# Optimization experiments

Hardware: AMD Instinct MI355X
Metric: run time of the kernel (lower is better)

Reference implementation:

```python
import jax, jax.numpy as jnp
import numpy as np
import math

N, S, D, C, CLASSES = 512, 256, 512, 1024, 1000


def setup_inputs() -> dict:
    key = jax.random.key(0)
    ks = jax.random.split(key, 9)
    q = jax.random.normal(ks[0], (N, D), dtype=jnp.float32)
    K = jax.random.normal(ks[1], (N, S, D), dtype=jnp.float32)
    V = jax.random.normal(ks[2], (N, S, D), dtype=jnp.float32)
    codebook = jax.random.normal(ks[3], (C, D), dtype=jnp.float32) / math.sqrt(D)
    Wq = jax.random.normal(ks[4], (D, D), dtype=jnp.float32) / math.sqrt(D)
    Wc = jax.random.normal(ks[5], (CLASSES, D), dtype=jnp.float32) / math.sqrt(D)
    bc = jnp.zeros((CLASSES,), dtype=jnp.float32)
    Wr = jax.random.normal(ks[6], (D, D), dtype=jnp.float32) / math.sqrt(D)
    br = jnp.zeros((D,), dtype=jnp.float32)
    return {"q": q, "K": K, "V": V, "codebook": codebook,
            "Wq": Wq, "Wc": Wc, "bc": bc, "Wr": Wr, "br": br}


def reference(q, K, V, codebook, Wq, Wc, bc, Wr, br):
    d = q.shape[-1]
    scale = math.sqrt(d)
    # query projection (Linear, no bias): q @ Wq^T
    q_proj = jnp.einsum('nd,ed->ne', q, Wq)
    # query-to-codebook soft assignment [n, c]
    code_weights = jax.nn.softmax(jnp.einsum('nd,cd->nc', q_proj, codebook) / scale, axis=-1)
    # slot-to-codebook soft assignment [n, s, c]
    slot_code_weights = jax.nn.softmax(jnp.einsum('nsd,cd->nsc', K, codebook) / scale, axis=-1)
    # fused: einsum('nc,ncd->nd', code_weights, einsum('nsc,nsd->ncd', ...))
    # == contract c first to get per-slot weights [n, s], then mix V.
    effective_weights = jnp.einsum('nc,nsc->ns', code_weights, slot_code_weights)
    summary = jnp.einsum('ns,nsd->nd', effective_weights, V)
    logits = jnp.einsum('nd,kd->nk', summary, Wc) + bc
    recon = jnp.einsum('nd,ed->ne', summary, Wr) + br
    return (logits, recon, effective_weights)
```

## Files before the change

kernel.cpp:

```cpp
#include <hip/hip_runtime.h>
#include <hip/hip_bf16.h>
#include <stdint.h>


typedef float  f32x4 __attribute__((ext_vector_type(4)));
typedef float  f32x2 __attribute__((ext_vector_type(2)));
typedef short  s16x8 __attribute__((ext_vector_type(8)));

__device__ __forceinline__ unsigned short f2bf(float x){
  unsigned u = __float_as_uint(x);
  u += 0x7fffu + ((u >> 16) & 1u);
  return (unsigned short)(u >> 16);
}
__device__ __forceinline__ float hsum4(f32x4 v){ return v[0]+v[1]+v[2]+v[3]; }

static constexpr float INV_SCALE = 0.04419417382415922f;

__global__ __launch_bounds__(256) void k_cbarr(const float* __restrict__ cb,
                                               unsigned short* __restrict__ cbB){
  const int g = blockIdx.x*256 + threadIdx.x;
  const int ks8 = g & 3;
  const int cr  = (g >> 2) & 31;
  const int kk  = (g >> 7) & 15;
  const int p   = g >> 11;
  const int c = p*32 + cr;
  const int k = kk*32 + ks8*8;
  const float* src = cb + (size_t)c*512 + k;
  const f32x4 v0 = *(const f32x4*)(src);
  const f32x4 v1 = *(const f32x4*)(src + 4);
  s16x8 o;
  o[0]=(short)f2bf(v0[0]*INV_SCALE); o[1]=(short)f2bf(v0[1]*INV_SCALE);
  o[2]=(short)f2bf(v0[2]*INV_SCALE); o[3]=(short)f2bf(v0[3]*INV_SCALE);
  o[4]=(short)f2bf(v1[0]*INV_SCALE); o[5]=(short)f2bf(v1[1]*INV_SCALE);
  o[6]=(short)f2bf(v1[2]*INV_SCALE); o[7]=(short)f2bf(v1[3]*INV_SCALE);
  *(s16x8*)(cbB + (size_t)g*8) = o;
}

__global__ __launch_bounds__(256) void k_cw(const float* __restrict__ q,
                                            const float* __restrict__ Wq,
                                            const float* __restrict__ cb,
                                            float* __restrict__ cw){
  __shared__ __align__(16) float qrow[2][512];
  __shared__ __align__(16) float qproj[2][512];
  __shared__ float ev[2][1024];
  __shared__ float red[256];
  __shared__ float tot[2];
  const int t = threadIdx.x;
  const int n0 = blockIdx.x*2;

  #pragma unroll
  for (int j = 0; j < 4; ++j){
    const int o = t + 256*j; const int ni = o >> 9, d = o & 511;
    qrow[ni][d] = q[(size_t)(n0+ni)*512 + d];
  }
  __syncthreads();

  {
    const f32x4* q0 = (const f32x4*)qrow[0];
    const f32x4* q1 = (const f32x4*)qrow[1];
    #pragma unroll 1
    for (int j = 0; j < 2; ++j){
      const int e = t + 256*j;
      const f32x4* w4 = (const f32x4*)(Wq + (size_t)e*512);
      f32x4 a0={0,0,0,0},a1={0,0,0,0};
      for (int d = 0; d < 128; ++d){
        const f32x4 wv = w4[d];
        a0 += wv*q0[d]; a1 += wv*q1[d];
      }
      qproj[0][e]=hsum4(a0); qproj[1][e]=hsum4(a1);
    }
  }
  __syncthreads();

  {
    const f32x4* p0 = (const f32x4*)qproj[0];
    const f32x4* p1 = (const f32x4*)qproj[1];
    #pragma unroll 1
    for (int j = 0; j < 4; ++j){
      const int c = t + 256*j;
      const f32x4* c4 = (const f32x4*)(cb + (size_t)c*512);
      f32x4 a0={0,0,0,0},a1={0,0,0,0};
      for (int d = 0; d < 128; ++d){
        const f32x4 wv = c4[d];
        a0 += wv*p0[d]; a1 += wv*p1[d];
      }
      ev[0][c] = __expf(hsum4(a0)*INV_SCALE);
      ev[1][c] = __expf(hsum4(a1)*INV_SCALE);
    }
  }
  __syncthreads();

  for (int ni = 0; ni < 2; ++ni){
    red[t] = ev[ni][t] + ev[ni][t+256] + ev[ni][t+512] + ev[ni][t+768];
    __syncthreads();
    for (int off = 128; off > 0; off >>= 1){
      if (t < off) red[t] += red[t+off];
      __syncthreads();
    }
    if (t == 0) tot[ni] = red[0];
    __syncthreads();
  }
  #pragma unroll
  for (int j = 0; j < 8; ++j){
    const int o = t + 256*j; const int ni = o >> 10, c = o & 1023;
    cw[(size_t)(n0+ni)*1024 + c] = ev[ni][c] / tot[ni];
  }
}

__global__ __launch_bounds__(512, 4) void k_scores(const float* __restrict__ Kt,
                                                   const unsigned short* __restrict__ cbB,
                                                   const float* __restrict__ cw,
                                                   float* __restrict__ ew_out){
  __shared__ __align__(16) short sA[64*512];
  __shared__ float cwl[1024];
  __shared__ float pe[8][64];
  __shared__ float pw[8][64];

  const int t    = threadIdx.x;
  const int lane = t & 63;
  const int w    = t >> 6;
  const int m0   = blockIdx.x * 64;
  const int n    = m0 >> 8;

  {
    const int row = t >> 3;
    const float* src = Kt + (size_t)(m0 + row) * 512;
    #pragma unroll
    for (int j = 0; j < 8; ++j){
      const int slot = (t & 7) + 8*j;
      const f32x4 v0 = *(const f32x4*)(src + slot*8);
      const f32x4 v1 = *(const f32x4*)(src + slot*8 + 4);
      s16x8 o;
      o[0]=(short)f2bf(v0[0]); o[1]=(short)f2bf(v0[1]); o[2]=(short)f2bf(v0[2]); o[3]=(short)f2bf(v0[3]);
      o[4]=(short)f2bf(v1[0]); o[5]=(short)f2bf(v1[1]); o[6]=(short)f2bf(v1[2]); o[7]=(short)f2bf(v1[3]);
      const int sp = slot ^ (row & 7);
      *(s16x8*)&sA[row*512 + sp*8] = o;
    }
  }
  cwl[t]       = cw[(size_t)n*1024 + t];
  cwl[t + 512] = cw[(size_t)n*1024 + t + 512];
  __syncthreads();

  const int kg = lane >> 4;
  const int lr = lane & 15;
  const int rot = blockIdx.x & 3;

  float es[4][4], ws[4][4];
  #pragma unroll
  for (int fr = 0; fr < 4; ++fr)
    #pragma unroll
    for (int r = 0; r < 4; ++r){ es[fr][r] = 0.f; ws[fr][r] = 0.f; }

  #pragma unroll 1
  for (int p = 0; p < 4; ++p){
    const int ci = (p + rot) & 3;
    f32x4 acc[4][2];
    #pragma unroll
    for (int fr = 0; fr < 4; ++fr)
      #pragma unroll
      for (int fc = 0; fc < 2; ++fc) acc[fr][fc] = (f32x4){0.f,0.f,0.f,0.f};

    const unsigned short* pbase = cbB + ((size_t)(ci*8 + w))*16384;
    const int loff = lr*32 + kg*8;

    s16x8 a[4], b[2][2];
    #pragma unroll
    for (int fc = 0; fc < 2; ++fc)
      b[0][fc] = *(const s16x8*)(pbase + 0*1024 + fc*512 + loff);
    #pragma unroll
    for (int fc = 0; fc < 2; ++fc)
      b[1][fc] = *(const s16x8*)(pbase + 1*1024 + fc*512 + loff);

    #pragma unroll
    for (int kk = 0; kk < 16; ++kk){
      if (kk < 15) asm volatile("s_waitcnt vmcnt(2)" ::: "memory");
      else         asm volatile("s_waitcnt vmcnt(0)" ::: "memory");
      __builtin_amdgcn_sched_barrier(0);
      #pragma unroll
      for (int fr = 0; fr < 4; ++fr){
        const int row = fr*16 + lr;
        const int sp  = (kk*4 + kg) ^ (row & 7);
        a[fr] = *(const s16x8*)&sA[row*512 + sp*8];
      }
      __builtin_amdgcn_s_setprio(1);
      #pragma unroll
      for (int fr = 0; fr < 4; ++fr)
        #pragma unroll
        for (int fc = 0; fc < 2; ++fc)
          acc[fr][fc] = __builtin_amdgcn_mfma_f32_16x16x32_bf16(a[fr], b[kk & 1][fc], acc[fr][fc], 0, 0, 0);
      __builtin_amdgcn_s_setprio(0);
      __builtin_amdgcn_sched_barrier(0);
      if (kk < 14){
        #pragma unroll
        for (int fc = 0; fc < 2; ++fc)
          b[kk & 1][fc] = *(const s16x8*)(pbase + (size_t)(kk+2)*1024 + fc*512 + loff);
      }
    }

    const float cwv0 = cwl[ci*256 + w*32 + 0*16 + lr];
    const float cwv1 = cwl[ci*256 + w*32 + 1*16 + lr];
    #pragma unroll
    for (int fr = 0; fr < 4; ++fr){
      #pragma unroll
      for (int r = 0; r < 4; ++r){
        const float e0 = __expf(acc[fr][0][r]);
        const float e1 = __expf(acc[fr][1][r]);
        es[fr][r] += e0 + e1;
        ws[fr][r] += e0 * cwv0 + e1 * cwv1;
      }
    }
  }

  #pragma unroll
  for (int fr = 0; fr < 4; ++fr){
    #pragma unroll
    for (int r = 0; r < 4; ++r){
      float a0 = es[fr][r], b0 = ws[fr][r];
      #pragma unroll
      for (int m = 1; m < 16; m <<= 1){
        a0 += __shfl_xor(a0, m, 64);
        b0 += __shfl_xor(b0, m, 64);
      }
      if (lr == 0){
        const int row = fr*16 + kg*4 + r;
        pe[w][row] = a0;
        pw[w][row] = b0;
      }
    }
  }

  __syncthreads();
  if (t < 64){
    float se = 0.f, sw = 0.f;
    #pragma unroll
    for (int i = 0; i < 8; ++i){ se += pe[i][t]; sw += pw[i][t]; }
    ew_out[m0 + t] = sw / se;
  }
}

__global__ __launch_bounds__(256) void k_summary(const float* __restrict__ V,
                                                 const float* __restrict__ ew,
                                                 float* __restrict__ sm){
  __shared__ float e[256];
  __shared__ f32x4 red[3][64];
  const int t = threadIdx.x;
  const int lane = t & 63, w = t >> 6;
  const int n = blockIdx.x >> 1;
  const int d0 = (blockIdx.x & 1) * 256;
  e[t] = ew[(size_t)n*256 + t];
  __syncthreads();
  const float* vb = V + (size_t)n*131072 + d0 + lane*4;
  f32x4 acc = {0.f,0.f,0.f,0.f};
  #pragma unroll 8
  for (int s = w; s < 256; s += 4){
    const f32x4 v = *(const f32x4*)(vb + (size_t)s*512);
    acc += e[s] * v;
  }
  if (w > 0) red[w-1][lane] = acc;
  __syncthreads();
  if (w == 0){
    acc += red[0][lane] + red[1][lane] + red[2][lane];
    *(f32x4*)(sm + (size_t)n*512 + d0 + lane*4) = acc;
  }
}

__global__ __launch_bounds__(256) void k_readout(const float* __restrict__ sm,
                                                 const float* __restrict__ Wc,
                                                 const float* __restrict__ bc,
                                                 const float* __restrict__ Wr,
                                                 const float* __restrict__ br,
                                                 float* __restrict__ logits,
                                                 float* __restrict__ recon){
  __shared__ __align__(16) float sl[8][512];
  const int t = threadIdx.x;
  const int nb  = blockIdx.x >> 2;
  const int wsl = blockIdx.x & 3;
  const int n0 = nb * 8;
  #pragma unroll
  for (int j = 0; j < 16; ++j){
    const int o = t + 256*j; const int ni = o >> 9, d = o & 511;
    sl[ni][d] = sm[(size_t)(n0+ni)*512 + d];
  }
  __syncthreads();
  #pragma unroll 1
  for (int j = 0; j < 2; ++j){
    const int rel = t + 256*j;
    if (rel >= 378) continue;
    const int o = wsl*378 + rel;
    const bool isl = o < 1000;
    const float* wrow = isl ? (Wc + (size_t)o*512) : (Wr + (size_t)(o-1000)*512);
    const float bias  = isl ? bc[o] : br[o-1000];
    const f32x4* w4 = (const f32x4*)wrow;
    f32x4 av[8];
    #pragma unroll
    for (int ni = 0; ni < 8; ++ni) av[ni] = (f32x4){0.f,0.f,0.f,0.f};
    for (int d = 0; d < 128; ++d){
      const f32x4 wv = w4[d];
      #pragma unroll
      for (int ni = 0; ni < 8; ++ni)
        av[ni] += wv * ((const f32x4*)sl[ni])[d];
    }
    #pragma unroll
    for (int ni = 0; ni < 8; ++ni){
      const float r = hsum4(av[ni]) + bias;
      if (isl) logits[(size_t)(n0+ni)*1000 + o] = r;
      else     recon [(size_t)(n0+ni)*512 + (o-1000)] = r;
    }
  }
}

extern "C" void kernel_launch(void* const* d_in, const int* in_sizes, int n_in,
                              void* d_out, int out_size, void* d_ws, size_t ws_size,
                              hipStream_t stream) {
  const float* q  = (const float*)d_in[0];
  const float* K  = (const float*)d_in[1];
  const float* V  = (const float*)d_in[2];
  const float* cb = (const float*)d_in[3];
  const float* Wq = (const float*)d_in[4];
  const float* Wc = (const float*)d_in[5];
  const float* bc = (const float*)d_in[6];
  const float* Wr = (const float*)d_in[7];
  const float* br = (const float*)d_in[8];

  float* out    = (float*)d_out;
  float* logits = out;
  float* recon  = out + 512*1000;
  float* ew     = out + 512*1000 + 512*512;

  char* wsb = (char*)d_ws;
  unsigned short* cbB = (unsigned short*)wsb;
  float* cw = (float*)(wsb + (1u<<20));
  float* sm = (float*)(wsb + 3u*(1u<<20));

  hipLaunchKernelGGL(k_cbarr,   dim3(256),  dim3(256), 0, stream, cb, cbB);
  hipLaunchKernelGGL(k_cw,      dim3(256),  dim3(256), 0, stream, q, Wq, cb, cw);
  hipLaunchKernelGGL(k_scores,  dim3(2048), dim3(512), 0, stream, K, cbB, cw, ew);
  hipLaunchKernelGGL(k_summary, dim3(1024), dim3(256), 0, stream, V, ew, sm);
  hipLaunchKernelGGL(k_readout, dim3(256),  dim3(256), 0, stream, sm, Wc, bc, Wr, br, logits, recon);
}
```

Before: 387.1 us.

## Fuse V-weighted summary into score kernel and merge prep kernels

Merges the codebook bf16 conversion and code-weight kernels into one launch, and fuses the weighted V reduction into the score kernel. Each score block writes a partial summary over its 64 slots, and the readout kernel sums four partials per row. This drops one launch plus the separate pass that reread effective weights, and it moves V streaming into the score kernel. The fused path depends on the workspace being large enough, otherwise it falls back to the old path, and it adds extra work to the score kernel tail.

```diff
diff --git a/kernel.cpp b/kernel.cpp
--- a/kernel.cpp
+++ b/kernel.cpp
@@ -16,45 +16,45 @@
 
 static constexpr float INV_SCALE = 0.04419417382415922f;
 
-__global__ __launch_bounds__(256) void k_cbarr(const float* __restrict__ cb,
-                                               unsigned short* __restrict__ cbB){
-  const int g = blockIdx.x*256 + threadIdx.x;
-  const int ks8 = g & 3;
-  const int cr  = (g >> 2) & 31;
-  const int kk  = (g >> 7) & 15;
-  const int p   = g >> 11;
-  const int c = p*32 + cr;
-  const int k = kk*32 + ks8*8;
-  const float* src = cb + (size_t)c*512 + k;
-  const f32x4 v0 = *(const f32x4*)(src);
-  const f32x4 v1 = *(const f32x4*)(src + 4);
-  s16x8 o;
-  o[0]=(short)f2bf(v0[0]*INV_SCALE); o[1]=(short)f2bf(v0[1]*INV_SCALE);
-  o[2]=(short)f2bf(v0[2]*INV_SCALE); o[3]=(short)f2bf(v0[3]*INV_SCALE);
-  o[4]=(short)f2bf(v1[0]*INV_SCALE); o[5]=(short)f2bf(v1[1]*INV_SCALE);
-  o[6]=(short)f2bf(v1[2]*INV_SCALE); o[7]=(short)f2bf(v1[3]*INV_SCALE);
-  *(s16x8*)(cbB + (size_t)g*8) = o;
-}
-
-__global__ __launch_bounds__(256) void k_cw(const float* __restrict__ q,
-                                            const float* __restrict__ Wq,
-                                            const float* __restrict__ cb,
-                                            float* __restrict__ cw){
+__global__ __launch_bounds__(256) void k_prep(const float* __restrict__ cb,
+                                              unsigned short* __restrict__ cbB,
+                                              const float* __restrict__ q,
+                                              const float* __restrict__ Wq,
+                                              float* __restrict__ cw){
   __shared__ __align__(16) float qrow[2][512];
   __shared__ __align__(16) float qproj[2][512];
   __shared__ float ev[2][1024];
   __shared__ float red[256];
   __shared__ float tot[2];
   const int t = threadIdx.x;
-  const int n0 = blockIdx.x*2;
-
+
+  if (blockIdx.x < 256){
+    const int g = blockIdx.x*256 + t;
+    const int ks8 = g & 3;
+    const int cr  = (g >> 2) & 31;
+    const int kk  = (g >> 7) & 15;
+    const int p   = g >> 11;
+    const int c = p*32 + cr;
+    const int k = kk*32 + ks8*8;
+    const float* src = cb + (size_t)c*512 + k;
+    const f32x4 v0 = *(const f32x4*)(src);
+    const f32x4 v1 = *(const f32x4*)(src + 4);
+    s16x8 o;
+    o[0]=(short)f2bf(v0[0]*INV_SCALE); o[1]=(short)f2bf(v0[1]*INV_SCALE);
+    o[2]=(short)f2bf(v0[2]*INV_SCALE); o[3]=(short)f2bf(v0[3]*INV_SCALE);
+    o[4]=(short)f2bf(v1[0]*INV_SCALE); o[5]=(short)f2bf(v1[1]*INV_SCALE);
+    o[6]=(short)f2bf(v1[2]*INV_SCALE); o[7]=(short)f2bf(v1[3]*INV_SCALE);
+    *(s16x8*)(cbB + (size_t)g*8) = o;
+    return;
+  }
+
+  const int n0 = (blockIdx.x - 256)*2;
   #pragma unroll
   for (int j = 0; j < 4; ++j){
     const int o = t + 256*j; const int ni = o >> 9, d = o & 511;
     qrow[ni][d] = q[(size_t)(n0+ni)*512 + d];
   }
   __syncthreads();
-
   {
     const f32x4* q0 = (const f32x4*)qrow[0];
     const f32x4* q1 = (const f32x4*)qrow[1];
@@ -71,7 +71,6 @@
     }
   }
   __syncthreads();
-
   {
     const f32x4* p0 = (const f32x4*)qproj[0];
     const f32x4* p1 = (const f32x4*)qproj[1];
@@ -89,7 +88,6 @@
     }
   }
   __syncthreads();
-
   for (int ni = 0; ni < 2; ++ni){
     red[t] = ev[ni][t] + ev[ni][t+256] + ev[ni][t+512] + ev[ni][t+768];
     __syncthreads();
@@ -107,14 +105,18 @@
   }
 }
 
+template<bool FUSE_V>
 __global__ __launch_bounds__(512, 4) void k_scores(const float* __restrict__ Kt,
                                                    const unsigned short* __restrict__ cbB,
                                                    const float* __restrict__ cw,
-                                                   float* __restrict__ ew_out){
+                                                   float* __restrict__ ew_out,
+                                                   const float* __restrict__ Vp,
+                                                   float* __restrict__ partial){
   __shared__ __align__(16) short sA[64*512];
   __shared__ float cwl[1024];
   __shared__ float pe[8][64];
   __shared__ float pw[8][64];
+  __shared__ float ewl[64];
 
   const int t    = threadIdx.x;
   const int lane = t & 63;
@@ -234,7 +236,33 @@
     float se = 0.f, sw = 0.f;
     #pragma unroll
     for (int i = 0; i < 8; ++i){ se += pe[i][t]; sw += pw[i][t]; }
-    ew_out[m0 + t] = sw / se;
+    const float e = sw / se;
+    ew_out[m0 + t] = e;
+    ewl[t] = e;
+  }
+
+  if constexpr (FUSE_V){
+    __syncthreads();
+    float* psum = (float*)sA;
+    const int sh = t >> 7;
+    const int dq = (t & 127) * 4;
+    const float* vb = Vp + (size_t)m0*512 + dq;
+    f32x4 av = {0.f,0.f,0.f,0.f};
+    #pragma unroll
+    for (int i = 0; i < 16; ++i){
+      const int s = sh*16 + i;
+      av += ewl[s] * *(const f32x4*)(vb + (size_t)s*512);
+    }
+    *(f32x4*)&psum[sh*512 + dq] = av;
+    __syncthreads();
+    if (t < 128){
+      const int d4 = t*4;
+      f32x4 r = *(f32x4*)&psum[d4];
+      r += *(f32x4*)&psum[512 + d4];
+      r += *(f32x4*)&psum[1024 + d4];
+      r += *(f32x4*)&psum[1536 + d4];
+      *(f32x4*)&partial[(size_t)blockIdx.x*512 + d4] = r;
+    }
   }
 }
 
@@ -264,7 +292,8 @@
   }
 }
 
-__global__ __launch_bounds__(256) void k_readout(const float* __restrict__ sm,
+template<bool FUSED>
+__global__ __launch_bounds__(256) void k_readout(const float* __restrict__ src,
                                                  const float* __restrict__ Wc,
                                                  const float* __restrict__ bc,
                                                  const float* __restrict__ Wr,
@@ -279,7 +308,12 @@
   #pragma unroll
   for (int j = 0; j < 16; ++j){
     const int o = t + 256*j; const int ni = o >> 9, d = o & 511;
-    sl[ni][d] = sm[(size_t)(n0+ni)*512 + d];
+    if (FUSED){
+      const float* pb = src + (size_t)(n0+ni)*2048 + d;
+      sl[ni][d] = pb[0] + pb[512] + pb[1024] + pb[1536];
+    } else {
+      sl[ni][d] = src[(size_t)(n0+ni)*512 + d];
+    }
   }
   __syncthreads();
   #pragma unroll 1
@@ -329,12 +363,18 @@
 
   char* wsb = (char*)d_ws;
   unsigned short* cbB = (unsigned short*)wsb;
-  float* cw = (float*)(wsb + (1u<<20));
-  float* sm = (float*)(wsb + 3u*(1u<<20));
-
-  hipLaunchKernelGGL(k_cbarr,   dim3(256),  dim3(256), 0, stream, cb, cbB);
-  hipLaunchKernelGGL(k_cw,      dim3(256),  dim3(256), 0, stream, q, Wq, cb, cw);
-  hipLaunchKernelGGL(k_scores,  dim3(2048), dim3(512), 0, stream, K, cbB, cw, ew);
-  hipLaunchKernelGGL(k_summary, dim3(1024), dim3(256), 0, stream, V, ew, sm);
-  hipLaunchKernelGGL(k_readout, dim3(256),  dim3(256), 0, stream, sm, Wc, bc, Wr, br, logits, recon);
-}
+  float* cw   = (float*)(wsb + (1u<<20));
+  float* aux  = (float*)(wsb + 3u*(1u<<20));
+
+  const bool fused = ws_size >= (size_t)(7u<<20);
+
+  k_prep<<<dim3(512), dim3(256), 0, stream>>>(cb, cbB, q, Wq, cw);
+  if (fused){
+    k_scores<true><<<dim3(2048), dim3(512), 0, stream>>>(K, cbB, cw, ew, V, aux);
+    k_readout<true><<<dim3(256), dim3(256), 0, stream>>>(aux, Wc, bc, Wr, br, logits, recon);
+  } else {
+    k_scores<false><<<dim3(2048), dim3(512), 0, stream>>>(K, cbB, cw, ew, V, aux);
+    k_summary<<<dim3(1024), dim3(256), 0, stream>>>(V, ew, aux);
+    k_readout<false><<<dim3(256), dim3(256), 0, stream>>>(aux, Wc, bc, Wr, br, logits, recon);
+  }
+}
```

Result: faster. 372.6 us (-3.8%).
